# Optimization experiments

Hardware: AMD Instinct MI355X
Metric: run time of the kernel (lower is better)

## Reference

```python
import jax, jax.numpy as jnp
import numpy as np

CENTER_LR = 0.5  # EMA learning rate for centers (init arg lr)


def setup_inputs() -> dict:
    key = jax.random.key(0)
    k1, k2, k3 = jax.random.split(key, 3)
    B, D, C = 131072, 256, 1000
    feats = jax.random.normal(k1, (B, D), dtype=jnp.float32)
    centers = jax.random.normal(k2, (C, D), dtype=jnp.float32)
    labels = jax.random.randint(k3, (B,), 0, C, dtype=jnp.int64)
    return {"feats": feats, "centers": centers, "labels": labels}


def reference(feats, centers, labels):
    # EMA center update (done under no_grad in the original):
    # for each class c present in the batch:
    #   centers[c] = (1-lr)*centers[c] + lr*mean(feats[labels==c])
    C = centers.shape[0]
    counts = jax.ops.segment_sum(jnp.ones(labels.shape, feats.dtype), labels,
                                 num_segments=C)                       # [C]
    sums = jax.ops.segment_sum(feats, labels, num_segments=C)          # [C, D]
    means = sums / jnp.maximum(counts, 1.0)[:, None]                   # [C, D]
    present = (counts > 0)[:, None]
    new_centers = jnp.where(present,
                            (1.0 - CENTER_LR) * centers + CENTER_LR * means,
                            centers)                                   # [C, D]
    new_centers = jax.lax.stop_gradient(new_centers)
    # loss = 0.5 * mean_i ||f_i - c_{y_i}||^2
    sel = new_centers[labels]                                          # [B, D]
    diff = feats - sel
    loss = 0.5 * jnp.mean(jnp.sum(diff * diff, axis=1))
    return loss
```

## Files before the change

kernel.cpp:

```cpp
#include <hip/hip_runtime.h>


#define DDIM 256
#define DDIM4 64


__global__ __launch_bounds__(1024) void k0_zero(int* __restrict__ counts,
                                                int* __restrict__ scal16) {
    int t = threadIdx.x;
    counts[t] = 0;
    if (t < 16) scal16[t] = 0;
}

__global__ __launch_bounds__(256) void k1_hist(const int* __restrict__ labels,
                                               int* __restrict__ counts,
                                               int B, int C) {
    __shared__ int h[1024];
    for (int i = threadIdx.x; i < 1024; i += 256) h[i] = 0;
    __syncthreads();
    int stride = gridDim.x * 256;
    for (int i = blockIdx.x * 256 + threadIdx.x; i < B; i += stride)
        atomicAdd(&h[labels[i]], 1);
    __syncthreads();
    for (int i = threadIdx.x; i < C; i += 256) {
        int v = h[i];
        if (v) atomicAdd(&counts[i], v);
    }
}

__global__ __launch_bounds__(1024) void k2_scan(const int* __restrict__ counts,
                                                int* __restrict__ offsets,
                                                int* __restrict__ cursor, int C) {
    __shared__ int sc[1024];
    int t = threadIdx.x;
    int mine = (t < C) ? counts[t] : 0;
    sc[t] = mine;
    __syncthreads();
    for (int off = 1; off < 1024; off <<= 1) {
        int add = (t >= off) ? sc[t - off] : 0;
        __syncthreads();
        sc[t] += add;
        __syncthreads();
    }
    if (t < C) {
        int e = sc[t] - mine;
        offsets[t] = e;
        cursor[t]  = e;
    }
}

__global__ __launch_bounds__(256) void k3_scatter(const int* __restrict__ labels,
                                                  int* __restrict__ cursor,
                                                  int* __restrict__ rowidx, int B) {
    int stride = gridDim.x * 256;
    for (int i = blockIdx.x * 256 + threadIdx.x; i < B; i += stride) {
        int c = labels[i];
        int pos = atomicAdd(&cursor[c], 1);
        rowidx[pos] = i;
    }
}

__global__ __launch_bounds__(256) void k4_class(const float4* __restrict__ feats4,
                                                const float* __restrict__ centers,
                                                const int* __restrict__ rowidx,
                                                const int* __restrict__ counts,
                                                const int* __restrict__ offsets,
                                                float* __restrict__ scalars,
                                                int* __restrict__ ticket,
                                                float* __restrict__ out,
                                                int nblocks, float invB) {
    __shared__ float comb[4 * DDIM];
    __shared__ float red[12];
    __shared__ int lastflag;

    int c = blockIdx.x;
    int count = counts[c];
    int start = offsets[c];
    int t = threadIdx.x, wave = t >> 6, lane = t & 63;

    int per = (count + 3) >> 2;
    int wbeg = wave * per;
    int wend = min(count, wbeg + per);

    float4 acc = make_float4(0.f, 0.f, 0.f, 0.f);
    float ff = 0.f;

    int i = wbeg;
    for (; i + 8 <= wend; i += 8) {
        int j[8];
        float4 v[8];
#pragma unroll
        for (int k = 0; k < 8; ++k) j[k] = rowidx[start + i + k];
#pragma unroll
        for (int k = 0; k < 8; ++k) v[k] = feats4[j[k] * DDIM4 + lane];
#pragma unroll
        for (int k = 0; k < 8; ++k) {
            acc.x += v[k].x; acc.y += v[k].y; acc.z += v[k].z; acc.w += v[k].w;
            ff += v[k].x*v[k].x + v[k].y*v[k].y + v[k].z*v[k].z + v[k].w*v[k].w;
        }
    }
    for (; i < wend; ++i) {
        float4 v = feats4[rowidx[start + i] * DDIM4 + lane];
        acc.x += v.x; acc.y += v.y; acc.z += v.z; acc.w += v.w;
        ff += v.x*v.x + v.y*v.y + v.z*v.z + v.w*v.w;
    }

    comb[wave * DDIM + lane * 4 + 0] = acc.x;
    comb[wave * DDIM + lane * 4 + 1] = acc.y;
    comb[wave * DDIM + lane * 4 + 2] = acc.z;
    comb[wave * DDIM + lane * 4 + 3] = acc.w;
    __syncthreads();

    float s  = comb[t] + comb[DDIM + t] + comb[2 * DDIM + t] + comb[3 * DDIM + t];
    float co = centers[c * DDIM + t];
    float nc = (count > 0) ? 0.5f * co + 0.5f * s / (float)count : co;
    float dotv = nc * s;
    float ccv  = nc * nc * (float)count;

#pragma unroll
    for (int off = 32; off > 0; off >>= 1) {
        ff   += __shfl_down(ff, off);
        dotv += __shfl_down(dotv, off);
        ccv  += __shfl_down(ccv, off);
    }
    if (lane == 0) {
        red[wave * 3 + 0] = ff;
        red[wave * 3 + 1] = dotv;
        red[wave * 3 + 2] = ccv;
    }
    __syncthreads();
    if (t == 0) {
        atomicAdd(&scalars[0], red[0] + red[3] + red[6] + red[9]);
        atomicAdd(&scalars[1], red[1] + red[4] + red[7] + red[10]);
        atomicAdd(&scalars[2], red[2] + red[5] + red[8] + red[11]);
        __threadfence();
        int old = atomicAdd(ticket, 1);
        lastflag = (old == nblocks - 1) ? 1 : 0;
    }
    __syncthreads();
    if (lastflag && t == 0) {
        __threadfence();
        float a = atomicAdd(&scalars[0], 0.f);
        float b = atomicAdd(&scalars[1], 0.f);
        float e = atomicAdd(&scalars[2], 0.f);
        out[0] = 0.5f * invB * (a - 2.f * b + e);
    }
}

extern "C" void kernel_launch(void* const* d_in, const int* in_sizes, int n_in,
                              void* d_out, int out_size, void* d_ws, size_t ws_size,
                              hipStream_t stream) {
    const float* feats   = (const float*)d_in[0];
    const float* centers = (const float*)d_in[1];
    const int*   labels  = (const int*)d_in[2];

    int B = in_sizes[2];
    int Dv = in_sizes[0] / B;
    int C = in_sizes[1] / Dv;
    (void)Dv; (void)n_in; (void)ws_size; (void)out_size;

    int* W = (int*)d_ws;
    int* counts    = W;
    int* offsets   = W + 1024;
    int* cursor    = W + 2048;
    float* scalars = (float*)(W + 3072);
    int* ticket    = W + 3072 + 12;
    int* rowidx    = W + 3072 + 16;

    k0_zero<<<1, 1024, 0, stream>>>(counts, W + 3072);
    k1_hist<<<256, 256, 0, stream>>>(labels, counts, B, C);
    k2_scan<<<1, 1024, 0, stream>>>(counts, offsets, cursor, C);
    int sblocks = (B + 255) / 256;
    if (sblocks > 512) sblocks = 512;
    k3_scatter<<<sblocks, 256, 0, stream>>>(labels, cursor, rowidx, B);
    k4_class<<<C, 256, 0, stream>>>((const float4*)feats, centers, rowidx,
                                    counts, offsets, scalars, ticket,
                                    (float*)d_out, C, 1.0f / (float)B);
}
```

Before: 116.8 us.

## Replace sort-and-gather segment sum with streaming LDS atomic accumulation

Drops the scan, scatter and per-class gather kernels. Feature rows are now streamed contiguously, and each block owns one 32-column slice of one row slab. Blocks accumulate per-class partial sums in a 1000x32 shared-memory table with LDS float atomics, then write the partials to workspace. A separate epilogue kernel reduces the 32 slab partials per class and computes the loss terms. This swaps random-row gathers and two serial kernels for coalesced reads, at the cost of heavy LDS atomic contention, a large shared table that limits occupancy, and extra partial traffic. The code assumes B divides evenly into slabs.

After: 238.7 us. 2.04x slower.

```diff
diff --git a/kernel.cpp b/kernel.cpp
--- a/kernel.cpp
+++ b/kernel.cpp
@@ -2,7 +2,10 @@
 
 
 #define DDIM 256
-#define DDIM4 64
+#define NSLICE 8
+#define SLABS 32
+#define TSTRIDE 36
+#define NCLASS_MAX 1000
 
 
 __global__ __launch_bounds__(1024) void k0_zero(int* __restrict__ counts,
@@ -28,122 +31,138 @@
     }
 }
 
-__global__ __launch_bounds__(1024) void k2_scan(const int* __restrict__ counts,
-                                                int* __restrict__ offsets,
-                                                int* __restrict__ cursor, int C) {
-    __shared__ int sc[1024];
-    int t = threadIdx.x;
-    int mine = (t < C) ? counts[t] : 0;
-    sc[t] = mine;
+__global__ __launch_bounds__(512) void k_stream(const float4* __restrict__ feats4,
+                                                const int* __restrict__ labels,
+                                                float* __restrict__ part,
+                                                float* __restrict__ scalars,
+                                                int B, int C) {
+    __shared__ float table[NCLASS_MAX * TSTRIDE];
+    __shared__ float red[8];
+
+    int s = blockIdx.x & 7;
+    int j = blockIdx.x >> 3;
+    int t = threadIdx.x, wave = t >> 6, lane = t & 63;
+
+    int tsz = C * TSTRIDE;
+    for (int i = t; i < tsz; i += 512) table[i] = 0.f;
     __syncthreads();
-    for (int off = 1; off < 1024; off <<= 1) {
-        int add = (t >= off) ? sc[t - off] : 0;
-        __syncthreads();
-        sc[t] += add;
-        __syncthreads();
+
+    int rows_per_slab = B / SLABS;
+    int rows_per_wave = rows_per_slab / 8;
+    int r0 = j * rows_per_slab + wave * rows_per_wave;
+
+    int rsub = lane >> 3;
+    int seg  = lane & 7;
+    float ff = 0.f;
+
+    const float4* fbase = feats4 + (size_t)s * 8 + seg;
+
+    int base = 0;
+    for (; base + 32 <= rows_per_wave; base += 32) {
+        int ra = r0 + base + rsub;
+        int rb = ra + 8, rc = ra + 16, rd = ra + 24;
+        float4 va = fbase[(size_t)ra * 64];
+        float4 vb = fbase[(size_t)rb * 64];
+        float4 vc = fbase[(size_t)rc * 64];
+        float4 vd = fbase[(size_t)rd * 64];
+        int ca = labels[ra], cb = labels[rb], cc = labels[rc], cd = labels[rd];
+
+        ff += va.x*va.x + va.y*va.y + va.z*va.z + va.w*va.w;
+        ff += vb.x*vb.x + vb.y*vb.y + vb.z*vb.z + vb.w*vb.w;
+        ff += vc.x*vc.x + vc.y*vc.y + vc.z*vc.z + vc.w*vc.w;
+        ff += vd.x*vd.x + vd.y*vd.y + vd.z*vd.z + vd.w*vd.w;
+
+        int ba = ca * TSTRIDE + seg * 4;
+        atomicAdd(&table[ba + 0], va.x); atomicAdd(&table[ba + 1], va.y);
+        atomicAdd(&table[ba + 2], va.z); atomicAdd(&table[ba + 3], va.w);
+        int bb = cb * TSTRIDE + seg * 4;
+        atomicAdd(&table[bb + 0], vb.x); atomicAdd(&table[bb + 1], vb.y);
+        atomicAdd(&table[bb + 2], vb.z); atomicAdd(&table[bb + 3], vb.w);
+        int bc = cc * TSTRIDE + seg * 4;
+        atomicAdd(&table[bc + 0], vc.x); atomicAdd(&table[bc + 1], vc.y);
+        atomicAdd(&table[bc + 2], vc.z); atomicAdd(&table[bc + 3], vc.w);
+        int bd = cd * TSTRIDE + seg * 4;
+        atomicAdd(&table[bd + 0], vd.x); atomicAdd(&table[bd + 1], vd.y);
+        atomicAdd(&table[bd + 2], vd.z); atomicAdd(&table[bd + 3], vd.w);
     }
-    if (t < C) {
-        int e = sc[t] - mine;
-        offsets[t] = e;
-        cursor[t]  = e;
+    for (; base + 8 <= rows_per_wave; base += 8) {
+        int ra = r0 + base + rsub;
+        float4 va = fbase[(size_t)ra * 64];
+        int ca = labels[ra];
+        ff += va.x*va.x + va.y*va.y + va.z*va.z + va.w*va.w;
+        int ba = ca * TSTRIDE + seg * 4;
+        atomicAdd(&table[ba + 0], va.x); atomicAdd(&table[ba + 1], va.y);
+        atomicAdd(&table[ba + 2], va.z); atomicAdd(&table[ba + 3], va.w);
+    }
+    __syncthreads();
+
+    int nchunk = C * 8;
+    for (int idx = t; idx < nchunk; idx += 512) {
+        int c = idx >> 3, q = idx & 7;
+        float4 v = *(const float4*)&table[c * TSTRIDE + q * 4];
+        size_t off = (((size_t)(s * C + c)) * SLABS + j) * 32 + q * 4;
+        *(float4*)&part[off] = v;
+    }
+
+#pragma unroll
+    for (int off = 32; off > 0; off >>= 1) ff += __shfl_down(ff, off);
+    if (lane == 0) red[wave] = ff;
+    __syncthreads();
+    if (t == 0) {
+        float a = 0.f;
+#pragma unroll
+        for (int w = 0; w < 8; ++w) a += red[w];
+        atomicAdd(&scalars[0], a);
     }
 }
 
-__global__ __launch_bounds__(256) void k3_scatter(const int* __restrict__ labels,
-                                                  int* __restrict__ cursor,
-                                                  int* __restrict__ rowidx, int B) {
-    int stride = gridDim.x * 256;
-    for (int i = blockIdx.x * 256 + threadIdx.x; i < B; i += stride) {
-        int c = labels[i];
-        int pos = atomicAdd(&cursor[c], 1);
-        rowidx[pos] = i;
+__global__ __launch_bounds__(512) void k_epi(const float* __restrict__ part,
+                                             const float* __restrict__ centers,
+                                             const int* __restrict__ counts,
+                                             float* __restrict__ scalars,
+                                             int* __restrict__ ticket,
+                                             float* __restrict__ out,
+                                             int C, float invB) {
+    __shared__ float red2[16];
+    int c = blockIdx.x;
+    int t = threadIdx.x, s = t >> 6, lane = t & 63;
+    int d = lane & 31, jh = lane >> 5;
+
+    const float* base = part + (((size_t)(s * C + c)) * SLABS) * 32;
+    float acc = 0.f;
+    for (int jj = jh; jj < SLABS; jj += 2) acc += base[jj * 32 + d];
+    acc += __shfl_xor(acc, 32);
+
+    int count = counts[c];
+    float dotv = 0.f, ccv = 0.f;
+    if (lane < 32) {
+        float co = centers[c * DDIM + s * 32 + d];
+        float nc = (count > 0) ? 0.5f * co + 0.5f * acc / (float)count : co;
+        dotv = nc * acc;
+        ccv  = nc * nc * (float)count;
     }
-}
-
-__global__ __launch_bounds__(256) void k4_class(const float4* __restrict__ feats4,
-                                                const float* __restrict__ centers,
-                                                const int* __restrict__ rowidx,
-                                                const int* __restrict__ counts,
-                                                const int* __restrict__ offsets,
-                                                float* __restrict__ scalars,
-                                                int* __restrict__ ticket,
-                                                float* __restrict__ out,
-                                                int nblocks, float invB) {
-    __shared__ float comb[4 * DDIM];
-    __shared__ float red[12];
-    __shared__ int lastflag;
-
-    int c = blockIdx.x;
-    int count = counts[c];
-    int start = offsets[c];
-    int t = threadIdx.x, wave = t >> 6, lane = t & 63;
-
-    int per = (count + 3) >> 2;
-    int wbeg = wave * per;
-    int wend = min(count, wbeg + per);
-
-    float4 acc = make_float4(0.f, 0.f, 0.f, 0.f);
-    float ff = 0.f;
-
-    int i = wbeg;
-    for (; i + 8 <= wend; i += 8) {
-        int j[8];
-        float4 v[8];
 #pragma unroll
-        for (int k = 0; k < 8; ++k) j[k] = rowidx[start + i + k];
-#pragma unroll
-        for (int k = 0; k < 8; ++k) v[k] = feats4[j[k] * DDIM4 + lane];
-#pragma unroll
-        for (int k = 0; k < 8; ++k) {
-            acc.x += v[k].x; acc.y += v[k].y; acc.z += v[k].z; acc.w += v[k].w;
-            ff += v[k].x*v[k].x + v[k].y*v[k].y + v[k].z*v[k].z + v[k].w*v[k].w;
-        }
-    }
-    for (; i < wend; ++i) {
-        float4 v = feats4[rowidx[start + i] * DDIM4 + lane];
-        acc.x += v.x; acc.y += v.y; acc.z += v.z; acc.w += v.w;
-        ff += v.x*v.x + v.y*v.y + v.z*v.z + v.w*v.w;
-    }
-
-    comb[wave * DDIM + lane * 4 + 0] = acc.x;
-    comb[wave * DDIM + lane * 4 + 1] = acc.y;
-    comb[wave * DDIM + lane * 4 + 2] = acc.z;
-    comb[wave * DDIM + lane * 4 + 3] = acc.w;
-    __syncthreads();
-
-    float s  = comb[t] + comb[DDIM + t] + comb[2 * DDIM + t] + comb[3 * DDIM + t];
-    float co = centers[c * DDIM + t];
-    float nc = (count > 0) ? 0.5f * co + 0.5f * s / (float)count : co;
-    float dotv = nc * s;
-    float ccv  = nc * nc * (float)count;
-
-#pragma unroll
-    for (int off = 32; off > 0; off >>= 1) {
-        ff   += __shfl_down(ff, off);
+    for (int off = 16; off > 0; off >>= 1) {
         dotv += __shfl_down(dotv, off);
         ccv  += __shfl_down(ccv, off);
     }
-    if (lane == 0) {
-        red[wave * 3 + 0] = ff;
-        red[wave * 3 + 1] = dotv;
-        red[wave * 3 + 2] = ccv;
-    }
+    if (lane == 0) { red2[s * 2] = dotv; red2[s * 2 + 1] = ccv; }
     __syncthreads();
     if (t == 0) {
-        atomicAdd(&scalars[0], red[0] + red[3] + red[6] + red[9]);
-        atomicAdd(&scalars[1], red[1] + red[4] + red[7] + red[10]);
-        atomicAdd(&scalars[2], red[2] + red[5] + red[8] + red[11]);
+        float dsum = 0.f, csum = 0.f;
+#pragma unroll
+        for (int w = 0; w < 8; ++w) { dsum += red2[w * 2]; csum += red2[w * 2 + 1]; }
+        atomicAdd(&scalars[1], dsum);
+        atomicAdd(&scalars[2], csum);
         __threadfence();
         int old = atomicAdd(ticket, 1);
-        lastflag = (old == nblocks - 1) ? 1 : 0;
-    }
-    __syncthreads();
-    if (lastflag && t == 0) {
-        __threadfence();
-        float a = atomicAdd(&scalars[0], 0.f);
-        float b = atomicAdd(&scalars[1], 0.f);
-        float e = atomicAdd(&scalars[2], 0.f);
-        out[0] = 0.5f * invB * (a - 2.f * b + e);
+        if (old == C - 1) {
+            __threadfence();
+            float A  = atomicAdd(&scalars[0], 0.f);
+            float Bv = atomicAdd(&scalars[1], 0.f);
+            float E  = atomicAdd(&scalars[2], 0.f);
+            out[0] = 0.5f * invB * (A - 2.f * Bv + E);
+        }
     }
 }
 
@@ -161,19 +180,14 @@
 
     int* W = (int*)d_ws;
     int* counts    = W;
-    int* offsets   = W + 1024;
-    int* cursor    = W + 2048;
-    float* scalars = (float*)(W + 3072);
-    int* ticket    = W + 3072 + 12;
-    int* rowidx    = W + 3072 + 16;
+    float* scalars = (float*)(W + 1024);
+    int* ticket    = W + 1024 + 12;
+    float* part    = (float*)(W + 1040);
 
-    k0_zero<<<1, 1024, 0, stream>>>(counts, W + 3072);
+    k0_zero<<<1, 1024, 0, stream>>>(counts, W + 1024);
     k1_hist<<<256, 256, 0, stream>>>(labels, counts, B, C);
-    k2_scan<<<1, 1024, 0, stream>>>(counts, offsets, cursor, C);
-    int sblocks = (B + 255) / 256;
-    if (sblocks > 512) sblocks = 512;
-    k3_scatter<<<sblocks, 256, 0, stream>>>(labels, cursor, rowidx, B);
-    k4_class<<<C, 256, 0, stream>>>((const float4*)feats, centers, rowidx,
-                                    counts, offsets, scalars, ticket,
-                                    (float*)d_out, C, 1.0f / (float)B);
+    k_stream<<<SLABS * NSLICE, 512, 0, stream>>>((const float4*)feats, labels,
+                                                 part, scalars, B, C);
+    k_epi<<<C, 512, 0, stream>>>(part, centers, counts, scalars, ticket,
+                                 (float*)d_out, C, 1.0f / (float)B);
 }
```

## Split per-class reduction into uniform row spans with atomic flush and epilogue

Applied to the files above, without the earlier changes.

The one-block-per-class accumulation kernel is replaced by a kernel where each wave handles a fixed span of 64 sorted rows and flushes partial class sums into a global sums buffer with float atomics when the label changes. A separate epilogue kernel computes the new centers and the loss terms per class. The histogram now writes per-block partial histograms, which the scan reduces, and it also zeroes the sums buffer, so the separate zeroing kernel is gone. The aim is to balance load across many more blocks instead of one block per class, at the cost of extra atomics, an extra launch and a round trip of the sums buffer through memory.

New measurement: 131.0 us. 1.12x slower.

```diff
diff --git a/kernel.cpp b/kernel.cpp
--- a/kernel.cpp
+++ b/kernel.cpp
@@ -2,39 +2,41 @@
 
 
 #define DDIM 256
-#define DDIM4 64
-
-
-__global__ __launch_bounds__(1024) void k0_zero(int* __restrict__ counts,
-                                                int* __restrict__ scal16) {
-    int t = threadIdx.x;
-    counts[t] = 0;
-    if (t < 16) scal16[t] = 0;
-}
+#define NHB 64
+#define HPAD 1024
+
 
 __global__ __launch_bounds__(256) void k1_hist(const int* __restrict__ labels,
-                                               int* __restrict__ counts,
+                                               int* __restrict__ hist_part,
+                                               float* __restrict__ sums,
+                                               float* __restrict__ scal16,
                                                int B, int C) {
     __shared__ int h[1024];
-    for (int i = threadIdx.x; i < 1024; i += 256) h[i] = 0;
+    int b = blockIdx.x, t = threadIdx.x;
+    for (int i = t; i < 1024; i += 256) h[i] = 0;
     __syncthreads();
-    int stride = gridDim.x * 256;
-    for (int i = blockIdx.x * 256 + threadIdx.x; i < B; i += stride)
-        atomicAdd(&h[labels[i]], 1);
+    int per = (B + NHB - 1) / NHB;
+    int base = b * per;
+    int end = min(B, base + per);
+    for (int i = base + t; i < end; i += 256) atomicAdd(&h[labels[i]], 1);
     __syncthreads();
-    for (int i = threadIdx.x; i < C; i += 256) {
-        int v = h[i];
-        if (v) atomicAdd(&counts[i], v);
-    }
-}
-
-__global__ __launch_bounds__(1024) void k2_scan(const int* __restrict__ counts,
+    for (int i = t; i < 1024; i += 256) hist_part[b * HPAD + i] = h[i];
+    int nf4 = C * (DDIM / 4);
+    float4* s4 = (float4*)sums;
+    float4 z = make_float4(0.f, 0.f, 0.f, 0.f);
+    for (int i = b * 256 + t; i < nf4; i += NHB * 256) s4[i] = z;
+    if (b == 0 && t < 16) scal16[t] = 0.f;
+}
+
+__global__ __launch_bounds__(1024) void k2_scan(const int* __restrict__ hist_part,
+                                                int* __restrict__ counts,
                                                 int* __restrict__ offsets,
                                                 int* __restrict__ cursor, int C) {
     __shared__ int sc[1024];
     int t = threadIdx.x;
-    int mine = (t < C) ? counts[t] : 0;
-    sc[t] = mine;
+    int v = 0;
+    for (int b = 0; b < NHB; ++b) v += hist_part[b * HPAD + t];
+    sc[t] = v;
     __syncthreads();
     for (int off = 1; off < 1024; off <<= 1) {
         int add = (t >= off) ? sc[t - off] : 0;
@@ -43,7 +45,8 @@
         __syncthreads();
     }
     if (t < C) {
-        int e = sc[t] - mine;
+        int e = sc[t] - v;
+        counts[t] = v;
         offsets[t] = e;
         cursor[t]  = e;
     }
@@ -60,90 +63,122 @@
     }
 }
 
-__global__ __launch_bounds__(256) void k4_class(const float4* __restrict__ feats4,
-                                                const float* __restrict__ centers,
-                                                const int* __restrict__ rowidx,
-                                                const int* __restrict__ counts,
-                                                const int* __restrict__ offsets,
-                                                float* __restrict__ scalars,
-                                                int* __restrict__ ticket,
-                                                float* __restrict__ out,
-                                                int nblocks, float invB) {
-    __shared__ float comb[4 * DDIM];
-    __shared__ float red[12];
-    __shared__ int lastflag;
-
-    int c = blockIdx.x;
-    int count = counts[c];
-    int start = offsets[c];
+__global__ __launch_bounds__(256) void k4_span(const float4* __restrict__ feats4,
+                                               const int* __restrict__ rowidx,
+                                               const int* __restrict__ labels,
+                                               float* __restrict__ sums,
+                                               float* __restrict__ scalars, int B) {
     int t = threadIdx.x, wave = t >> 6, lane = t & 63;
-
-    int per = (count + 3) >> 2;
-    int wbeg = wave * per;
-    int wend = min(count, wbeg + per);
+    int g = blockIdx.x * 4 + wave;
+    int start = g * 64;
+    if (start >= B) return;
+    int n = min(64, B - start);
+
+    int p = start + ((lane < n) ? lane : (n - 1));
+    int ridx = rowidx[p];
+    int lbl  = labels[ridx];
 
     float4 acc = make_float4(0.f, 0.f, 0.f, 0.f);
     float ff = 0.f;
-
-    int i = wbeg;
-    for (; i + 8 <= wend; i += 8) {
-        int j[8];
-        float4 v[8];
+    int cur = __shfl(lbl, 0);
+
+#define FLUSH() do { float* bp = &sums[cur * DDIM + lane * 4];              \
+        atomicAdd(bp + 0, acc.x); atomicAdd(bp + 1, acc.y);                 \
+        atomicAdd(bp + 2, acc.z); atomicAdd(bp + 3, acc.w); } while (0)
+
+#define ROWK(IDX, V) { int ck = __shfl(lbl, (IDX));                         \
+        if (ck != cur) { FLUSH(); acc = make_float4(0.f,0.f,0.f,0.f); cur = ck; } \
+        acc.x += V.x; acc.y += V.y; acc.z += V.z; acc.w += V.w; }
+
+    if (n == 64) {
+        for (int i = 0; i < 64; i += 8) {
+            int r0 = __shfl(ridx, i + 0), r1 = __shfl(ridx, i + 1);
+            int r2 = __shfl(ridx, i + 2), r3 = __shfl(ridx, i + 3);
+            int r4 = __shfl(ridx, i + 4), r5 = __shfl(ridx, i + 5);
+            int r6 = __shfl(ridx, i + 6), r7 = __shfl(ridx, i + 7);
+            float4 v0 = feats4[r0 * 64 + lane];
+            float4 v1 = feats4[r1 * 64 + lane];
+            float4 v2 = feats4[r2 * 64 + lane];
+            float4 v3 = feats4[r3 * 64 + lane];
+            float4 v4 = feats4[r4 * 64 + lane];
+            float4 v5 = feats4[r5 * 64 + lane];
+            float4 v6 = feats4[r6 * 64 + lane];
+            float4 v7 = feats4[r7 * 64 + lane];
+
+            ff += v0.x*v0.x + v0.y*v0.y + v0.z*v0.z + v0.w*v0.w;
+            ff += v1.x*v1.x + v1.y*v1.y + v1.z*v1.z + v1.w*v1.w;
+            ff += v2.x*v2.x + v2.y*v2.y + v2.z*v2.z + v2.w*v2.w;
+            ff += v3.x*v3.x + v3.y*v3.y + v3.z*v3.z + v3.w*v3.w;
+            ff += v4.x*v4.x + v4.y*v4.y + v4.z*v4.z + v4.w*v4.w;
+            ff += v5.x*v5.x + v5.y*v5.y + v5.z*v5.z + v5.w*v5.w;
+            ff += v6.x*v6.x + v6.y*v6.y + v6.z*v6.z + v6.w*v6.w;
+            ff += v7.x*v7.x + v7.y*v7.y + v7.z*v7.z + v7.w*v7.w;
+
+            int c0 = __shfl(lbl, i + 0), c7 = __shfl(lbl, i + 7);
+            if (c0 == cur && c7 == cur) {
+                acc.x += v0.x + v1.x + v2.x + v3.x + v4.x + v5.x + v6.x + v7.x;
+                acc.y += v0.y + v1.y + v2.y + v3.y + v4.y + v5.y + v6.y + v7.y;
+                acc.z += v0.z + v1.z + v2.z + v3.z + v4.z + v5.z + v6.z + v7.z;
+                acc.w += v0.w + v1.w + v2.w + v3.w + v4.w + v5.w + v6.w + v7.w;
+            } else {
+                ROWK(i + 0, v0); ROWK(i + 1, v1); ROWK(i + 2, v2); ROWK(i + 3, v3);
+                ROWK(i + 4, v4); ROWK(i + 5, v5); ROWK(i + 6, v6); ROWK(i + 7, v7);
+            }
+        }
+    } else {
+        for (int i = 0; i < n; ++i) {
+            int r = __shfl(ridx, i);
+            float4 v = feats4[r * 64 + lane];
+            ff += v.x*v.x + v.y*v.y + v.z*v.z + v.w*v.w;
+            ROWK(i, v);
+        }
+    }
+    FLUSH();
+
 #pragma unroll
-        for (int k = 0; k < 8; ++k) j[k] = rowidx[start + i + k];
-#pragma unroll
-        for (int k = 0; k < 8; ++k) v[k] = feats4[j[k] * DDIM4 + lane];
-#pragma unroll
-        for (int k = 0; k < 8; ++k) {
-            acc.x += v[k].x; acc.y += v[k].y; acc.z += v[k].z; acc.w += v[k].w;
-            ff += v[k].x*v[k].x + v[k].y*v[k].y + v[k].z*v[k].z + v[k].w*v[k].w;
-        }
-    }
-    for (; i < wend; ++i) {
-        float4 v = feats4[rowidx[start + i] * DDIM4 + lane];
-        acc.x += v.x; acc.y += v.y; acc.z += v.z; acc.w += v.w;
-        ff += v.x*v.x + v.y*v.y + v.z*v.z + v.w*v.w;
-    }
-
-    comb[wave * DDIM + lane * 4 + 0] = acc.x;
-    comb[wave * DDIM + lane * 4 + 1] = acc.y;
-    comb[wave * DDIM + lane * 4 + 2] = acc.z;
-    comb[wave * DDIM + lane * 4 + 3] = acc.w;
-    __syncthreads();
-
-    float s  = comb[t] + comb[DDIM + t] + comb[2 * DDIM + t] + comb[3 * DDIM + t];
-    float co = centers[c * DDIM + t];
-    float nc = (count > 0) ? 0.5f * co + 0.5f * s / (float)count : co;
-    float dotv = nc * s;
-    float ccv  = nc * nc * (float)count;
+    for (int off = 32; off > 0; off >>= 1) ff += __shfl_xor(ff, off);
+    if (lane == 0) atomicAdd(&scalars[0], ff);
+#undef ROWK
+#undef FLUSH
+}
+
+__global__ __launch_bounds__(64) void k_epi(const float* __restrict__ sums,
+                                            const float* __restrict__ centers,
+                                            const int* __restrict__ counts,
+                                            float* __restrict__ scalars,
+                                            int* __restrict__ ticket,
+                                            float* __restrict__ out,
+                                            int C, float invB) {
+    int c = blockIdx.x, lane = threadIdx.x;
+    float4 s  = *(const float4*)&sums[c * DDIM + lane * 4];
+    float4 co = *(const float4*)&centers[c * DDIM + lane * 4];
+    int n = counts[c];
+    float inv = (n > 0) ? 0.5f / (float)n : 0.f;
+    float4 nc;
+    nc.x = 0.5f * co.x + s.x * inv;
+    nc.y = 0.5f * co.y + s.y * inv;
+    nc.z = 0.5f * co.z + s.z * inv;
+    nc.w = 0.5f * co.w + s.w * inv;
+    float dotv = nc.x * s.x + nc.y * s.y + nc.z * s.z + nc.w * s.w;
+    float ccv  = (nc.x*nc.x + nc.y*nc.y + nc.z*nc.z + nc.w*nc.w) * (float)n;
 
 #pragma unroll
     for (int off = 32; off > 0; off >>= 1) {
-        ff   += __shfl_down(ff, off);
         dotv += __shfl_down(dotv, off);
         ccv  += __shfl_down(ccv, off);
     }
     if (lane == 0) {
-        red[wave * 3 + 0] = ff;
-        red[wave * 3 + 1] = dotv;
-        red[wave * 3 + 2] = ccv;
-    }
-    __syncthreads();
-    if (t == 0) {
-        atomicAdd(&scalars[0], red[0] + red[3] + red[6] + red[9]);
-        atomicAdd(&scalars[1], red[1] + red[4] + red[7] + red[10]);
-        atomicAdd(&scalars[2], red[2] + red[5] + red[8] + red[11]);
+        atomicAdd(&scalars[1], dotv);
+        atomicAdd(&scalars[2], ccv);
         __threadfence();
         int old = atomicAdd(ticket, 1);
-        lastflag = (old == nblocks - 1) ? 1 : 0;
-    }
-    __syncthreads();
-    if (lastflag && t == 0) {
-        __threadfence();
-        float a = atomicAdd(&scalars[0], 0.f);
-        float b = atomicAdd(&scalars[1], 0.f);
-        float e = atomicAdd(&scalars[2], 0.f);
-        out[0] = 0.5f * invB * (a - 2.f * b + e);
+        if (old == C - 1) {
+            __threadfence();
+            float A  = atomicAdd(&scalars[0], 0.f);
+            float Bv = atomicAdd(&scalars[1], 0.f);
+            float E  = atomicAdd(&scalars[2], 0.f);
+            out[0] = 0.5f * invB * (A - 2.f * Bv + E);
+        }
     }
 }
 
@@ -165,15 +200,18 @@
     int* cursor    = W + 2048;
     float* scalars = (float*)(W + 3072);
     int* ticket    = W + 3072 + 12;
-    int* rowidx    = W + 3072 + 16;
-
-    k0_zero<<<1, 1024, 0, stream>>>(counts, W + 3072);
-    k1_hist<<<256, 256, 0, stream>>>(labels, counts, B, C);
-    k2_scan<<<1, 1024, 0, stream>>>(counts, offsets, cursor, C);
+    int* hist_part = W + 3072 + 16;
+    float* sums    = (float*)(hist_part + NHB * HPAD);
+    int* rowidx    = (int*)(sums + C * DDIM);
+
+    k1_hist<<<NHB, 256, 0, stream>>>(labels, hist_part, sums, scalars, B, C);
+    k2_scan<<<1, 1024, 0, stream>>>(hist_part, counts, offsets, cursor, C);
     int sblocks = (B + 255) / 256;
     if (sblocks > 512) sblocks = 512;
     k3_scatter<<<sblocks, 256, 0, stream>>>(labels, cursor, rowidx, B);
-    k4_class<<<C, 256, 0, stream>>>((const float4*)feats, centers, rowidx,
-                                    counts, offsets, scalars, ticket,
-                                    (float*)d_out, C, 1.0f / (float)B);
-}
+    int gblocks = (B + 255) / 256;
+    k4_span<<<gblocks, 256, 0, stream>>>((const float4*)feats, rowidx, labels,
+                                         sums, scalars, B);
+    k_epi<<<C, 64, 0, stream>>>(sums, centers, counts, scalars, ticket,
+                                (float*)d_out, C, 1.0f / (float)B);
+}
```
